# Performance work log

Measured on AMD Instinct MI355X. Metric: run time of the kernel, lower is better.

Reference implementation:

```python
import jax, jax.numpy as jnp
import numpy as np

B, S, D, H, E, K = 4, 1024, 1024, 4096, 8, 2


def setup_inputs() -> dict:
    key = jax.random.key(0)
    ks = jax.random.split(key, 5)
    std = 0.02
    return {
        "x": jax.random.normal(ks[0], (B, S, D), dtype=jnp.float32),
        "router_W": jax.random.normal(ks[1], (D, E), dtype=jnp.float32) * std,
        "W_in": jax.random.normal(ks[2], (E, D, H), dtype=jnp.float32) * std,
        "b_in": jnp.zeros((E, H), dtype=jnp.float32),
        "W_out": jax.random.normal(ks[3], (E, H, D), dtype=jnp.float32) * std,
        "b_out": jnp.zeros((E, D), dtype=jnp.float32),
    }


def reference(x, router_W, W_in, b_in, W_out, b_out):
    # ---- routing ----
    logits = jnp.einsum("bsd,de->bse", x, router_W)          # [B,S,E]
    probs = jax.nn.softmax(logits, axis=-1)                    # [B,S,E]
    top_p, top_i = jax.lax.top_k(probs, K)                     # [B,S,K]
    top_p = top_p / (jnp.sum(top_p, axis=-1, keepdims=True) + 1e-8)
    one_hot = jax.nn.one_hot(top_i, E, dtype=x.dtype)          # [B,S,K,E]
    combine = jnp.sum(one_hot * top_p[..., None], axis=-2)     # [B,S,E] per-expert weight

    # ---- experts (original runs full batch through every selected expert;
    #      with E=8, K=2 all experts are active, so run all densely) ----
    h = jnp.einsum("bsd,edh->ebsh", x, W_in) + b_in[:, None, None, :]
    h = jax.nn.gelu(h, approximate=False)
    y = jnp.einsum("ebsh,ehd->ebsd", h, W_out) + b_out[:, None, None, :]
    out = jnp.einsum("bse,ebsd->bsd", combine, y)              # weighted combine

    # ---- load-balancing aux loss ----
    expert_usage = jnp.mean(one_hot, axis=(0, 1, 2))           # f_i, fraction of routed slots
    avg_probs = jnp.mean(probs, axis=(0, 1))                   # P_i
    aux_loss = E * jnp.sum(avg_probs * expert_usage)
    return out, aux_loss
```

## Files before the change

kernel.cpp:

```cpp
#include <hip/hip_runtime.h>
#include <hip/hip_bf16.h>
#include <math.h>

#define B_ 4
#define S_ 1024
#define T_ (B_ * S_)
#define D_ 1024
#define H_ 4096
#define E_ 8
#define K_ 2
#define A_ (T_ * K_)
#define NTM_ 40

typedef __bf16 bf16x8_t __attribute__((ext_vector_type(8)));
typedef float f32x4_t __attribute__((ext_vector_type(4)));
typedef unsigned short u16x8_t __attribute__((ext_vector_type(8)));

__device__ inline unsigned short f2bf(float f) {
    __hip_bfloat16 h = __float2bfloat16(f);
    return *reinterpret_cast<unsigned short*>(&h);
}

__device__ __forceinline__ void gl2lds16(const unsigned short* g, unsigned short* l) {
    auto* gp = reinterpret_cast<const __attribute__((address_space(1))) unsigned int*>(
        reinterpret_cast<uintptr_t>(g));
    auto* lp = reinterpret_cast<__attribute__((address_space(3))) unsigned int*>(
        reinterpret_cast<uintptr_t>(l));
    __builtin_amdgcn_global_load_lds(gp, lp, 16, 0, 0);
}


__global__ void router_kernel(const float* __restrict__ x, const float* __restrict__ rw,
                              int* __restrict__ tok_e, float* __restrict__ tok_w,
                              int* __restrict__ counts_pad, float* __restrict__ probs_pad) {
    __shared__ float s_probs[E_];
    __shared__ int s_counts[E_];
    const int tid = threadIdx.x;
    if (tid < E_) { s_probs[tid] = 0.f; s_counts[tid] = 0; }
    __syncthreads();
    const int wave = tid >> 6;
    const int lane = tid & 63;

    float wprob[E_];
    int wcount[E_];
#pragma unroll
    for (int e = 0; e < E_; ++e) { wprob[e] = 0.f; wcount[e] = 0; }

    for (int tt = 0; tt < 4; ++tt) {
        const int token = blockIdx.x * 16 + wave * 4 + tt;
        const float* xr = x + (long)token * D_;
        float acc[E_];
#pragma unroll
        for (int e = 0; e < E_; ++e) acc[e] = 0.f;
        for (int i = 0; i < D_ / 64; ++i) {
            int d = i * 64 + lane;
            float xv = xr[d];
            const float* w = rw + (long)d * E_;
#pragma unroll
            for (int e = 0; e < E_; ++e) acc[e] += xv * w[e];
        }
#pragma unroll
        for (int e = 0; e < E_; ++e) {
            for (int off = 32; off > 0; off >>= 1)
                acc[e] += __shfl_down(acc[e], off);
        }
        if (lane == 0) {
            float m = acc[0];
            for (int e = 1; e < E_; ++e) m = fmaxf(m, acc[e]);
            float p[E_], s = 0.f;
            for (int e = 0; e < E_; ++e) { p[e] = expf(acc[e] - m); s += p[e]; }
            float inv = 1.f / s;
            for (int e = 0; e < E_; ++e) { p[e] *= inv; wprob[e] += p[e]; }
            int i0 = 0;
            for (int e = 1; e < E_; ++e) if (p[e] > p[i0]) i0 = e;
            int i1 = (i0 == 0) ? 1 : 0;
            for (int e = 0; e < E_; ++e) if (e != i0 && p[e] > p[i1]) i1 = e;
            float w0 = p[i0], w1 = p[i1];
            float inv2 = 1.f / (w0 + w1 + 1e-8f);
            tok_e[token * 2] = i0;
            tok_e[token * 2 + 1] = i1;
            tok_w[token * 2] = w0 * inv2;
            tok_w[token * 2 + 1] = w1 * inv2;
            wcount[i0]++; wcount[i1]++;
        }
    }
    if (lane == 0) {
#pragma unroll
        for (int e = 0; e < E_; ++e) {
            atomicAdd(&s_probs[e], wprob[e]);
            if (wcount[e]) atomicAdd(&s_counts[e], wcount[e]);
        }
    }
    __syncthreads();
    if (tid < E_) {
        atomicAdd(&probs_pad[tid * 32], s_probs[tid]);
        if (s_counts[tid]) atomicAdd(&counts_pad[tid * 32], s_counts[tid]);
    }
}

__global__ void offsets_aux_kernel(const int* __restrict__ counts_pad,
                                   const float* __restrict__ probs_pad,
                                   int* __restrict__ offsets,
                                   int* __restrict__ tile_e, int* __restrict__ tile_m,
                                   int* __restrict__ n_tiles, float* __restrict__ aux_out) {
    if (threadIdx.x == 0 && blockIdx.x == 0) {
        int run = 0, t = 0;
        for (int e = 0; e < E_; ++e) {
            int c = counts_pad[e * 32];
            offsets[e] = run;
            for (int m0 = 0; m0 < c; m0 += 256) {
                tile_e[t] = e; tile_m[t] = m0; ++t;
            }
            run += c;
        }
        offsets[E_] = run;
        *n_tiles = t;
        float aux = 0.f;
        for (int e = 0; e < E_; ++e)
            aux += (probs_pad[e * 32] / (float)T_) * ((float)counts_pad[e * 32] / (float)A_);
        *aux_out = (float)E_ * aux;
    }
}

__global__ void scatter_kernel(const int* __restrict__ tok_e, const float* __restrict__ tok_w,
                               const int* __restrict__ offsets, int* __restrict__ cursors_pad,
                               int* __restrict__ perm_token, float* __restrict__ perm_weight,
                               int* __restrict__ inv_pos) {
    int i = blockIdx.x * blockDim.x + threadIdx.x;
    int lane = threadIdx.x & 63;
    int e = tok_e[i];
    float w = tok_w[i];
    unsigned long long bal[E_];
#pragma unroll
    for (int q = 0; q < E_; ++q) bal[q] = __ballot(e == q);
    unsigned long long below = (1ull << lane) - 1ull;
    int rank = __popcll(bal[e] & below);
    int base = 0;
    if (lane < E_) {
        int c = __popcll(bal[lane]);
        if (c) base = atomicAdd(&cursors_pad[lane * 32], c);
    }
    int mybase = __shfl(base, e);
    int pos = offsets[e] + mybase + rank;
    perm_token[pos] = i >> 1;
    perm_weight[pos] = w;
    inv_pos[i] = pos;
}

__global__ void cast_x_kernel(const float* __restrict__ x, unsigned short* __restrict__ xb) {
    long i = (long)blockIdx.x * blockDim.x + threadIdx.x;
    float4 v = reinterpret_cast<const float4*>(x)[i];
    unsigned long long packed = (unsigned long long)f2bf(v.x)
        | ((unsigned long long)f2bf(v.y) << 16)
        | ((unsigned long long)f2bf(v.z) << 32)
        | ((unsigned long long)f2bf(v.w) << 48);
    reinterpret_cast<unsigned long long*>(xb)[i] = packed;
}

__global__ void transpose_cast_kernel(const float* __restrict__ in, unsigned short* __restrict__ out,
                                      int R, int C) {
    __shared__ float tile[64][65];
    const long e = blockIdx.z;
    const float* in_e = in + e * (long)R * C;
    unsigned short* out_e = out + e * (long)R * C;
    const int c0 = blockIdx.x * 64;
    const int r0 = blockIdx.y * 64;
    const int tid = threadIdx.x;
    const int c4 = (tid & 15) * 4;
    const int rb = tid >> 4;
#pragma unroll
    for (int i = 0; i < 4; ++i) {
        const int r = rb + i * 16;
        const float4 v = *reinterpret_cast<const float4*>(&in_e[(long)(r0 + r) * C + c0 + c4]);
        tile[r][c4] = v.x; tile[r][c4 + 1] = v.y; tile[r][c4 + 2] = v.z; tile[r][c4 + 3] = v.w;
    }
    __syncthreads();
    const int rs = (tid & 7) * 8;
    const int cb = tid >> 3;
#pragma unroll
    for (int i = 0; i < 2; ++i) {
        const int c = cb + i * 32;
        u16x8_t p;
#pragma unroll
        for (int j = 0; j < 8; ++j) p[j] = f2bf(tile[rs + j][c]);
        *reinterpret_cast<u16x8_t*>(&out_e[(long)(c0 + c) * R + r0 + rs]) = p;
    }
}

template <int PHASE, int NSPLIT>
__launch_bounds__(512, 2)
__global__ void moe_gemm_kernel(const unsigned short* __restrict__ A_src,
                                const unsigned short* __restrict__ B_src,
                                const float* __restrict__ bias,
                                const int* __restrict__ offsets,
                                const int* __restrict__ tile_e, const int* __restrict__ tile_m,
                                const int* __restrict__ p_ntiles,
                                const int* __restrict__ perm_token,
                                const float* __restrict__ perm_weight,
                                unsigned short* __restrict__ h_buf,
                                float* __restrict__ y_perm) {
    constexpr int Ksz  = (PHASE == 1) ? D_ : H_;
    constexpr int Kloc = (PHASE == 1) ? D_ : (H_ / NSPLIT);
    constexpr int Nsz  = (PHASE == 1) ? H_ : D_;
    constexpr int NT   = Kloc / 64;
    constexpr int NTN  = Nsz / 128;

    const int nwg = gridDim.x;
    const int id = blockIdx.x;
    const int q = nwg >> 3, r8 = nwg & 7;
    const int xcd = id & 7, sub = id >> 3;
    const int wg = (xcd < r8 ? xcd * (q + 1) : r8 * (q + 1) + (xcd - r8) * q) + sub;
    const int mt = wg % NTM_;
    if (mt >= *p_ntiles) return;
    const int rest = wg / NTM_;
    const int nt = rest % NTN;
    const int kh = rest / NTN;
    const int e = tile_e[mt];
    const int m0 = tile_m[mt];
    const int off_e = offsets[e];
    const int n_e = offsets[e + 1] - off_e;
    const int n0 = nt * 128;
    const long k_base = (long)kh * Kloc;

    __shared__ __attribute__((aligned(16))) unsigned short lds_a[3 * 256 * 64];
    __shared__ __attribute__((aligned(16))) unsigned short lds_b[3 * 128 * 64];

    const int tid = threadIdx.x;
    const int lane = tid & 63;
    const int wave = tid >> 6;
    const int wr = wave >> 1;
    const int wc = wave & 1;
    const int lrow = lane & 15;
    const int kg = lane >> 4;

    const unsigned short* gA[4];
    const unsigned short* gB[2];
    int dstA[4], dstB[2];
#pragma unroll
    for (int j = 0; j < 4; ++j) {
        const int chunk = j * 512 + tid;
        const int rr = chunk >> 3;
        const int ch = tid & 7;
        const int m_loc = m0 + rr;
        const int m_cl = (m_loc < n_e) ? m_loc : (n_e - 1);
        const int pos = off_e + m_cl;
        long arow;
        if (PHASE == 1) arow = (long)perm_token[pos] * Ksz;
        else            arow = (long)pos * Ksz;
        gA[j] = A_src + arow + k_base + ((ch ^ (rr & 7)) * 8);
        dstA[j] = (j * 512 + wave * 64) * 8;
    }
#pragma unroll
    for (int j = 0; j < 2; ++j) {
        const int chunk = j * 512 + tid;
        const int rr = chunk >> 3;
        const int ch = tid & 7;
        gB[j] = B_src + (long)e * Nsz * Ksz + (long)(n0 + rr) * Ksz + k_base + ((ch ^ (rr & 7)) * 8);
        dstB[j] = (j * 512 + wave * 64) * 8;
    }

    int aoff[2][4], boff[2][4];
#pragma unroll
    for (int kf = 0; kf < 2; ++kf)
#pragma unroll
        for (int i = 0; i < 4; ++i) {
            const int r = wr * 64 + i * 16 + lrow;
            aoff[kf][i] = r * 64 + (((kf * 4 + kg) ^ (r & 7)) * 8);
            const int c = wc * 64 + i * 16 + lrow;
            boff[kf][i] = c * 64 + (((kf * 4 + kg) ^ (c & 7)) * 8);
        }

    f32x4_t acc[4][4];
#pragma unroll
    for (int i = 0; i < 4; ++i)
#pragma unroll
        for (int j = 0; j < 4; ++j) acc[i][j] = (f32x4_t){0.f, 0.f, 0.f, 0.f};

#pragma unroll
    for (int tt = 0; tt < 2; ++tt) {
        gl2lds16(gA[0] + tt * 64, lds_a + tt * 16384 + dstA[0]);
        gl2lds16(gA[1] + tt * 64, lds_a + tt * 16384 + dstA[1]);
        gl2lds16(gB[0] + tt * 64, lds_b + tt * 8192 + dstB[0]);
        gl2lds16(gA[2] + tt * 64, lds_a + tt * 16384 + dstA[2]);
        gl2lds16(gA[3] + tt * 64, lds_a + tt * 16384 + dstA[3]);
        gl2lds16(gB[1] + tt * 64, lds_b + tt * 8192 + dstB[1]);
    }
    asm volatile("s_waitcnt vmcnt(6)" ::: "memory");
    __builtin_amdgcn_s_barrier();

    for (int t = 0; t < NT; ++t) {
        const int s = t % 3;
        const int s2 = (t + 2) % 3;
        const unsigned short* la = lds_a + s * 16384;
        const unsigned short* lb = lds_b + s * 8192;
        const bool pf = (t + 2 < NT);

        bf16x8_t a0[4], b0[4];
#pragma unroll
        for (int i = 0; i < 4; ++i) a0[i] = *reinterpret_cast<const bf16x8_t*>(la + aoff[0][i]);
#pragma unroll
        for (int i = 0; i < 4; ++i) b0[i] = *reinterpret_cast<const bf16x8_t*>(lb + boff[0][i]);
        if (pf) {
            gl2lds16(gA[0] + (t + 2) * 64, lds_a + s2 * 16384 + dstA[0]);
            gl2lds16(gA[1] + (t + 2) * 64, lds_a + s2 * 16384 + dstA[1]);
            gl2lds16(gB[0] + (t + 2) * 64, lds_b + s2 * 8192 + dstB[0]);
        }
        __builtin_amdgcn_s_barrier();
        asm volatile("s_waitcnt lgkmcnt(0)" ::: "memory");
        __builtin_amdgcn_sched_barrier(0);
        __builtin_amdgcn_s_setprio(1);
#pragma unroll
        for (int i = 0; i < 4; ++i)
#pragma unroll
            for (int j = 0; j < 4; ++j)
                acc[i][j] = __builtin_amdgcn_mfma_f32_16x16x32_bf16(a0[i], b0[j], acc[i][j], 0, 0, 0);
        __builtin_amdgcn_s_setprio(0);
        __builtin_amdgcn_s_barrier();

        bf16x8_t a1[4], b1[4];
#pragma unroll
        for (int i = 0; i < 4; ++i) a1[i] = *reinterpret_cast<const bf16x8_t*>(la + aoff[1][i]);
#pragma unroll
        for (int i = 0; i < 4; ++i) b1[i] = *reinterpret_cast<const bf16x8_t*>(lb + boff[1][i]);
        if (pf) {
            gl2lds16(gA[2] + (t + 2) * 64, lds_a + s2 * 16384 + dstA[2]);
            gl2lds16(gA[3] + (t + 2) * 64, lds_a + s2 * 16384 + dstA[3]);
            gl2lds16(gB[1] + (t + 2) * 64, lds_b + s2 * 8192 + dstB[1]);
        }
        __builtin_amdgcn_s_barrier();
        asm volatile("s_waitcnt lgkmcnt(0)" ::: "memory");
        __builtin_amdgcn_sched_barrier(0);
        __builtin_amdgcn_s_setprio(1);
#pragma unroll
        for (int i = 0; i < 4; ++i)
#pragma unroll
            for (int j = 0; j < 4; ++j)
                acc[i][j] = __builtin_amdgcn_mfma_f32_16x16x32_bf16(a1[i], b1[j], acc[i][j], 0, 0, 0);
        __builtin_amdgcn_s_setprio(0);
        if (t + 1 < NT) {
            if (t + 2 < NT) asm volatile("s_waitcnt vmcnt(6)" ::: "memory");
            else            asm volatile("s_waitcnt vmcnt(0)" ::: "memory");
        }
        __builtin_amdgcn_s_barrier();
    }

    const float* bias_e = bias + (long)e * Nsz;
    if (PHASE == 1) {
#pragma unroll
        for (int i = 0; i < 4; ++i) {
#pragma unroll
            for (int rq = 0; rq < 4; ++rq) {
                const int row_loc = wr * 64 + i * 16 + kg * 4 + rq;
                const int m_loc = m0 + row_loc;
                if (m_loc >= n_e) continue;
                const int pos = off_e + m_loc;
#pragma unroll
                for (int j = 0; j < 4; ++j) {
                    const int n = n0 + wc * 64 + j * 16 + lrow;
                    float v = acc[i][j][rq] + bias_e[n];
                    v = 0.5f * v * (1.0f + erff(v * 0.70710678118654752440f));
                    h_buf[(long)pos * Nsz + n] = f2bf(v);
                }
            }
        }
    } else {
        float* yp = y_perm + (long)kh * ((long)A_ * D_);
#pragma unroll
        for (int i = 0; i < 4; ++i) {
#pragma unroll
            for (int rq = 0; rq < 4; ++rq) {
                const int row_loc = wr * 64 + i * 16 + kg * 4 + rq;
                const int m_loc = m0 + row_loc;
                if (m_loc >= n_e) continue;
                const int pos = off_e + m_loc;
                const float wgt = perm_weight[pos];
#pragma unroll
                for (int j = 0; j < 4; ++j) {
                    const int n = n0 + wc * 64 + j * 16 + lrow;
                    float v = acc[i][j][rq] + ((kh == 0) ? bias_e[n] : 0.f);
                    yp[(long)pos * Nsz + n] = v * wgt;
                }
            }
        }
    }
}

__global__ void combine_kernel(const float* __restrict__ y_perm, const int* __restrict__ inv_pos,
                               float* __restrict__ out, int splitk) {
    int t = blockIdx.x;
    int d4 = threadIdx.x;
    int p0 = inv_pos[t * 2];
    int p1 = inv_pos[t * 2 + 1];
    const float4* y0 = reinterpret_cast<const float4*>(y_perm);
    float4 a = y0[(long)p0 * (D_ / 4) + d4];
    float4 b = y0[(long)p1 * (D_ / 4) + d4];
    float4 o = {a.x + b.x, a.y + b.y, a.z + b.z, a.w + b.w};
    if (splitk) {
        const float4* y1 = reinterpret_cast<const float4*>(y_perm + (long)A_ * D_);
        float4 c = y1[(long)p0 * (D_ / 4) + d4];
        float4 d = y1[(long)p1 * (D_ / 4) + d4];
        o.x += c.x + d.x; o.y += c.y + d.y; o.z += c.z + d.z; o.w += c.w + d.w;
    }
    reinterpret_cast<float4*>(out + (long)t * D_)[d4] = o;
}

extern "C" void kernel_launch(void* const* d_in, const int* in_sizes, int n_in,
                              void* d_out, int out_size, void* d_ws, size_t ws_size,
                              hipStream_t stream) {
    const float* x        = (const float*)d_in[0];
    const float* router_W = (const float*)d_in[1];
    const float* W_in     = (const float*)d_in[2];
    const float* b_in     = (const float*)d_in[3];
    const float* W_out    = (const float*)d_in[4];
    const float* b_out    = (const float*)d_in[5];
    float* out = (float*)d_out;

    char* ws = (char*)d_ws;
    size_t off = 0;
    auto alloc = [&](size_t bytes) -> void* {
        void* p = ws + off;
        off += (bytes + 255) & ~(size_t)255;
        return p;
    };

    const int splitk = (ws_size >= (size_t)290 * 1024 * 1024) ? 1 : 0;

    char* ctrl = (char*)alloc(4096);
    int* counts_pad   = (int*)ctrl;
    float* probs_pad  = (float*)(ctrl + 1024);
    int* cursors_pad  = (int*)(ctrl + 2048);
    int* offsets      = (int*)(ctrl + 3072);
    int* tile_e       = (int*)(ctrl + 3200);
    int* tile_m       = (int*)(ctrl + 3584);
    int* n_tiles      = (int*)(ctrl + 3968);
    int* tok_e         = (int*)alloc((size_t)A_ * 4);
    float* tok_w       = (float*)alloc((size_t)A_ * 4);
    int* perm_token    = (int*)alloc((size_t)A_ * 4);
    float* perm_weight = (float*)alloc((size_t)A_ * 4);
    int* inv_pos       = (int*)alloc((size_t)A_ * 4);
    unsigned short* x_bf    = (unsigned short*)alloc((size_t)T_ * D_ * 2);
    unsigned short* w_in_t  = (unsigned short*)alloc((size_t)E_ * D_ * H_ * 2);
    unsigned short* w_out_t = (unsigned short*)alloc((size_t)E_ * D_ * H_ * 2);
    unsigned short* h_buf   = (unsigned short*)alloc((size_t)A_ * H_ * 2);
    float* y_perm           = (float*)alloc((size_t)(1 + splitk) * A_ * D_ * 4);

    hipMemsetAsync(ctrl, 0, 4096, stream);

    cast_x_kernel<<<(T_ * D_ / 4) / 256, 256, 0, stream>>>(x, x_bf);
    transpose_cast_kernel<<<dim3(H_ / 64, D_ / 64, E_), 256, 0, stream>>>(W_in, w_in_t, D_, H_);
    transpose_cast_kernel<<<dim3(D_ / 64, H_ / 64, E_), 256, 0, stream>>>(W_out, w_out_t, H_, D_);
    router_kernel<<<T_ / 16, 256, 0, stream>>>(x, router_W, tok_e, tok_w, counts_pad, probs_pad);
    offsets_aux_kernel<<<1, 64, 0, stream>>>(counts_pad, probs_pad, offsets,
                                             tile_e, tile_m, n_tiles, out + (out_size - 1));
    scatter_kernel<<<A_ / 256, 256, 0, stream>>>(tok_e, tok_w, offsets, cursors_pad,
                                                 perm_token, perm_weight, inv_pos);

    moe_gemm_kernel<1, 1><<<NTM_ * (H_ / 128), 512, 0, stream>>>(
        x_bf, w_in_t, b_in, offsets, tile_e, tile_m, n_tiles,
        perm_token, perm_weight, h_buf, y_perm);
    if (splitk) {
        moe_gemm_kernel<2, 2><<<NTM_ * (D_ / 128) * 2, 512, 0, stream>>>(
            h_buf, w_out_t, b_out, offsets, tile_e, tile_m, n_tiles,
            perm_token, perm_weight, h_buf, y_perm);
    } else {
        moe_gemm_kernel<2, 1><<<NTM_ * (D_ / 128), 512, 0, stream>>>(
            h_buf, w_out_t, b_out, offsets, tile_e, tile_m, n_tiles,
            perm_token, perm_weight, h_buf, y_perm);
    }
    combine_kernel<<<T_, 256, 0, stream>>>(y_perm, inv_pos, out, splitk);
}
```

Before: 682.7 us.

## Widen GEMM N-tile to 256 with 32-wide K stages and new LDS swizzle

The MoE GEMM kernel is templated on the N-tile width. Both phases now use 256x256 output tiles, with waves arranged 2x4 instead of 4x2, while the split-K=1 fallback keeps 128. The K step per pipeline stage drops from 64 to 32, which halves the triple-buffered LDS footprint, and it uses a new XOR swizzle with per-wave 16-row load groups. Several intra-iteration barriers are removed, so one barrier per K step remains. The aim is more reuse of A and B per block and less synchronisation. The cost is twice as many K iterations, higher accumulator register pressure, and a slightly lower workspace threshold for split-K.

```diff
diff --git a/kernel.cpp b/kernel.cpp
--- a/kernel.cpp
+++ b/kernel.cpp
@@ -28,7 +28,6 @@
         reinterpret_cast<uintptr_t>(l));
     __builtin_amdgcn_global_load_lds(gp, lp, 16, 0, 0);
 }
-
 
 __global__ void router_kernel(const float* __restrict__ x, const float* __restrict__ rw,
                               int* __restrict__ tok_e, float* __restrict__ tok_w,
@@ -187,7 +186,7 @@
     }
 }
 
-template <int PHASE, int NSPLIT>
+template <int PHASE, int BN_, int NSPLIT>
 __launch_bounds__(512, 2)
 __global__ void moe_gemm_kernel(const unsigned short* __restrict__ A_src,
                                 const unsigned short* __restrict__ B_src,
@@ -200,10 +199,20 @@
                                 unsigned short* __restrict__ h_buf,
                                 float* __restrict__ y_perm) {
     constexpr int Ksz  = (PHASE == 1) ? D_ : H_;
-    constexpr int Kloc = (PHASE == 1) ? D_ : (H_ / NSPLIT);
+    constexpr int Kloc = Ksz / NSPLIT;
     constexpr int Nsz  = (PHASE == 1) ? H_ : D_;
-    constexpr int NT   = Kloc / 64;
-    constexpr int NTN  = Nsz / 128;
+    constexpr int NT   = Kloc / 32;
+    constexpr int NTN  = Nsz / BN_;
+    constexpr int WN   = BN_ / 64;
+    constexpr int WM   = 8 / WN;
+    constexpr int MROWS = 256 / WM;
+    constexpr int MF   = MROWS / 16;
+    constexpr int MH   = MF / 2;
+    constexpr int AI   = 2;
+    constexpr int BI   = BN_ / 128;
+    constexpr int SI   = AI + BI;
+    constexpr int ABUF = 256 * 32;
+    constexpr int BBUF = BN_ * 32;
 
     const int nwg = gridDim.x;
     const int id = blockIdx.x;
@@ -219,138 +228,118 @@
     const int m0 = tile_m[mt];
     const int off_e = offsets[e];
     const int n_e = offsets[e + 1] - off_e;
-    const int n0 = nt * 128;
+    const int n0 = nt * BN_;
     const long k_base = (long)kh * Kloc;
 
-    __shared__ __attribute__((aligned(16))) unsigned short lds_a[3 * 256 * 64];
-    __shared__ __attribute__((aligned(16))) unsigned short lds_b[3 * 128 * 64];
+    __shared__ __attribute__((aligned(16))) unsigned short lds_a[3 * ABUF];
+    __shared__ __attribute__((aligned(16))) unsigned short lds_b[3 * BBUF];
 
     const int tid = threadIdx.x;
     const int lane = tid & 63;
     const int wave = tid >> 6;
-    const int wr = wave >> 1;
-    const int wc = wave & 1;
+    const int wr = wave / WN;
+    const int wc = wave % WN;
     const int lrow = lane & 15;
     const int kg = lane >> 4;
 
-    const unsigned short* gA[4];
-    const unsigned short* gB[2];
-    int dstA[4], dstB[2];
-#pragma unroll
-    for (int j = 0; j < 4; ++j) {
-        const int chunk = j * 512 + tid;
-        const int rr = chunk >> 3;
-        const int ch = tid & 7;
-        const int m_loc = m0 + rr;
+    const int srow = lane >> 2;
+    const int sch  = (lane & 3) ^ ((lane >> 3) & 3);
+    const unsigned short* gA[AI];
+    const unsigned short* gB[BI];
+#pragma unroll
+    for (int j = 0; j < AI; ++j) {
+        const int g = wave * AI + j;
+        const int m_loc = m0 + g * 16 + srow;
         const int m_cl = (m_loc < n_e) ? m_loc : (n_e - 1);
         const int pos = off_e + m_cl;
         long arow;
         if (PHASE == 1) arow = (long)perm_token[pos] * Ksz;
         else            arow = (long)pos * Ksz;
-        gA[j] = A_src + arow + k_base + ((ch ^ (rr & 7)) * 8);
-        dstA[j] = (j * 512 + wave * 64) * 8;
-    }
-#pragma unroll
-    for (int j = 0; j < 2; ++j) {
-        const int chunk = j * 512 + tid;
-        const int rr = chunk >> 3;
-        const int ch = tid & 7;
-        gB[j] = B_src + (long)e * Nsz * Ksz + (long)(n0 + rr) * Ksz + k_base + ((ch ^ (rr & 7)) * 8);
-        dstB[j] = (j * 512 + wave * 64) * 8;
-    }
-
-    int aoff[2][4], boff[2][4];
-#pragma unroll
-    for (int kf = 0; kf < 2; ++kf)
-#pragma unroll
-        for (int i = 0; i < 4; ++i) {
-            const int r = wr * 64 + i * 16 + lrow;
-            aoff[kf][i] = r * 64 + (((kf * 4 + kg) ^ (r & 7)) * 8);
-            const int c = wc * 64 + i * 16 + lrow;
-            boff[kf][i] = c * 64 + (((kf * 4 + kg) ^ (c & 7)) * 8);
-        }
-
-    f32x4_t acc[4][4];
-#pragma unroll
-    for (int i = 0; i < 4; ++i)
+        gA[j] = A_src + arow + k_base + sch * 8;
+    }
+#pragma unroll
+    for (int j = 0; j < BI; ++j) {
+        const int g = wave * BI + j;
+        gB[j] = B_src + (long)e * Nsz * Ksz + (long)(n0 + g * 16 + srow) * Ksz + k_base + sch * 8;
+    }
+
+    const int rch = (kg ^ ((lrow >> 1) & 3)) * 8;
+    const int abase = (wr * MROWS + lrow) * 32 + rch;
+    const int bbase = (wc * 64 + lrow) * 32 + rch;
+
+    f32x4_t acc[MF][4];
+#pragma unroll
+    for (int i = 0; i < MF; ++i)
 #pragma unroll
         for (int j = 0; j < 4; ++j) acc[i][j] = (f32x4_t){0.f, 0.f, 0.f, 0.f};
 
 #pragma unroll
     for (int tt = 0; tt < 2; ++tt) {
-        gl2lds16(gA[0] + tt * 64, lds_a + tt * 16384 + dstA[0]);
-        gl2lds16(gA[1] + tt * 64, lds_a + tt * 16384 + dstA[1]);
-        gl2lds16(gB[0] + tt * 64, lds_b + tt * 8192 + dstB[0]);
-        gl2lds16(gA[2] + tt * 64, lds_a + tt * 16384 + dstA[2]);
-        gl2lds16(gA[3] + tt * 64, lds_a + tt * 16384 + dstA[3]);
-        gl2lds16(gB[1] + tt * 64, lds_b + tt * 8192 + dstB[1]);
-    }
-    asm volatile("s_waitcnt vmcnt(6)" ::: "memory");
+#pragma unroll
+        for (int j = 0; j < AI; ++j)
+            gl2lds16(gA[j] + tt * 32, lds_a + tt * ABUF + (wave * AI + j) * 512);
+#pragma unroll
+        for (int j = 0; j < BI; ++j)
+            gl2lds16(gB[j] + tt * 32, lds_b + tt * BBUF + (wave * BI + j) * 512);
+    }
+    if constexpr (SI == 4) asm volatile("s_waitcnt vmcnt(4)" ::: "memory");
+    else                   asm volatile("s_waitcnt vmcnt(3)" ::: "memory");
     __builtin_amdgcn_s_barrier();
 
+    int s = 0;
     for (int t = 0; t < NT; ++t) {
-        const int s = t % 3;
-        const int s2 = (t + 2) % 3;
-        const unsigned short* la = lds_a + s * 16384;
-        const unsigned short* lb = lds_b + s * 8192;
+        const int s2 = (s + 2 >= 3) ? s - 1 : s + 2;
+        const unsigned short* la = lds_a + s * ABUF;
+        const unsigned short* lb = lds_b + s * BBUF;
         const bool pf = (t + 2 < NT);
 
-        bf16x8_t a0[4], b0[4];
-#pragma unroll
-        for (int i = 0; i < 4; ++i) a0[i] = *reinterpret_cast<const bf16x8_t*>(la + aoff[0][i]);
-#pragma unroll
-        for (int i = 0; i < 4; ++i) b0[i] = *reinterpret_cast<const bf16x8_t*>(lb + boff[0][i]);
-        if (pf) {
-            gl2lds16(gA[0] + (t + 2) * 64, lds_a + s2 * 16384 + dstA[0]);
-            gl2lds16(gA[1] + (t + 2) * 64, lds_a + s2 * 16384 + dstA[1]);
-            gl2lds16(gB[0] + (t + 2) * 64, lds_b + s2 * 8192 + dstB[0]);
-        }
-        __builtin_amdgcn_s_barrier();
-        asm volatile("s_waitcnt lgkmcnt(0)" ::: "memory");
-        __builtin_amdgcn_sched_barrier(0);
-        __builtin_amdgcn_s_setprio(1);
-#pragma unroll
-        for (int i = 0; i < 4; ++i)
-#pragma unroll
-            for (int j = 0; j < 4; ++j)
-                acc[i][j] = __builtin_amdgcn_mfma_f32_16x16x32_bf16(a0[i], b0[j], acc[i][j], 0, 0, 0);
-        __builtin_amdgcn_s_setprio(0);
-        __builtin_amdgcn_s_barrier();
-
-        bf16x8_t a1[4], b1[4];
-#pragma unroll
-        for (int i = 0; i < 4; ++i) a1[i] = *reinterpret_cast<const bf16x8_t*>(la + aoff[1][i]);
-#pragma unroll
-        for (int i = 0; i < 4; ++i) b1[i] = *reinterpret_cast<const bf16x8_t*>(lb + boff[1][i]);
-        if (pf) {
-            gl2lds16(gA[2] + (t + 2) * 64, lds_a + s2 * 16384 + dstA[2]);
-            gl2lds16(gA[3] + (t + 2) * 64, lds_a + s2 * 16384 + dstA[3]);
-            gl2lds16(gB[1] + (t + 2) * 64, lds_b + s2 * 8192 + dstB[1]);
-        }
-        __builtin_amdgcn_s_barrier();
-        asm volatile("s_waitcnt lgkmcnt(0)" ::: "memory");
-        __builtin_amdgcn_sched_barrier(0);
-        __builtin_amdgcn_s_setprio(1);
-#pragma unroll
-        for (int i = 0; i < 4; ++i)
-#pragma unroll
-            for (int j = 0; j < 4; ++j)
-                acc[i][j] = __builtin_amdgcn_mfma_f32_16x16x32_bf16(a1[i], b1[j], acc[i][j], 0, 0, 0);
-        __builtin_amdgcn_s_setprio(0);
+        bf16x8_t b_frag[4];
+#pragma unroll
+        for (int p = 0; p < 2; ++p) {
+            bf16x8_t a_frag[MH];
+#pragma unroll
+            for (int f = 0; f < MH; ++f)
+                a_frag[f] = *reinterpret_cast<const bf16x8_t*>(la + abase + (p * MH + f) * 512);
+            if (p == 0) {
+#pragma unroll
+                for (int j = 0; j < 4; ++j)
+                    b_frag[j] = *reinterpret_cast<const bf16x8_t*>(lb + bbase + j * 512);
+            }
+            if (pf) {
+                gl2lds16(gA[p] + (t + 2) * 32, lds_a + s2 * ABUF + (wave * AI + p) * 512);
+                if (p < BI)
+                    gl2lds16(gB[p] + (t + 2) * 32, lds_b + s2 * BBUF + (wave * BI + p) * 512);
+            }
+            asm volatile("s_waitcnt lgkmcnt(0)" ::: "memory");
+            __builtin_amdgcn_sched_barrier(0);
+            __builtin_amdgcn_s_setprio(1);
+#pragma unroll
+            for (int f = 0; f < MH; ++f)
+#pragma unroll
+                for (int j = 0; j < 4; ++j)
+                    acc[p * MH + f][j] = __builtin_amdgcn_mfma_f32_16x16x32_bf16(
+                        a_frag[f], b_frag[j], acc[p * MH + f][j], 0, 0, 0);
+            __builtin_amdgcn_s_setprio(0);
+        }
         if (t + 1 < NT) {
-            if (t + 2 < NT) asm volatile("s_waitcnt vmcnt(6)" ::: "memory");
-            else            asm volatile("s_waitcnt vmcnt(0)" ::: "memory");
-        }
-        __builtin_amdgcn_s_barrier();
+            if (pf) {
+                if constexpr (SI == 4) asm volatile("s_waitcnt vmcnt(4)" ::: "memory");
+                else                   asm volatile("s_waitcnt vmcnt(3)" ::: "memory");
+            } else {
+                asm volatile("s_waitcnt vmcnt(0)" ::: "memory");
+            }
+            __builtin_amdgcn_s_barrier();
+        }
+        s = (s + 1 >= 3) ? 0 : s + 1;
     }
 
     const float* bias_e = bias + (long)e * Nsz;
     if (PHASE == 1) {
 #pragma unroll
-        for (int i = 0; i < 4; ++i) {
+        for (int i = 0; i < MF; ++i) {
 #pragma unroll
             for (int rq = 0; rq < 4; ++rq) {
-                const int row_loc = wr * 64 + i * 16 + kg * 4 + rq;
+                const int row_loc = wr * MROWS + i * 16 + kg * 4 + rq;
                 const int m_loc = m0 + row_loc;
                 if (m_loc >= n_e) continue;
                 const int pos = off_e + m_loc;
@@ -366,10 +355,10 @@
     } else {
         float* yp = y_perm + (long)kh * ((long)A_ * D_);
 #pragma unroll
-        for (int i = 0; i < 4; ++i) {
+        for (int i = 0; i < MF; ++i) {
 #pragma unroll
             for (int rq = 0; rq < 4; ++rq) {
-                const int row_loc = wr * 64 + i * 16 + kg * 4 + rq;
+                const int row_loc = wr * MROWS + i * 16 + kg * 4 + rq;
                 const int m_loc = m0 + row_loc;
                 if (m_loc >= n_e) continue;
                 const int pos = off_e + m_loc;
@@ -423,7 +412,7 @@
         return p;
     };
 
-    const int splitk = (ws_size >= (size_t)290 * 1024 * 1024) ? 1 : 0;
+    const int splitk = (ws_size >= (size_t)280 * 1024 * 1024) ? 1 : 0;
 
     char* ctrl = (char*)alloc(4096);
     int* counts_pad   = (int*)ctrl;
@@ -455,15 +444,15 @@
     scatter_kernel<<<A_ / 256, 256, 0, stream>>>(tok_e, tok_w, offsets, cursors_pad,
                                                  perm_token, perm_weight, inv_pos);
 
-    moe_gemm_kernel<1, 1><<<NTM_ * (H_ / 128), 512, 0, stream>>>(
+    moe_gemm_kernel<1, 256, 1><<<NTM_ * (H_ / 256), 512, 0, stream>>>(
         x_bf, w_in_t, b_in, offsets, tile_e, tile_m, n_tiles,
         perm_token, perm_weight, h_buf, y_perm);
     if (splitk) {
-        moe_gemm_kernel<2, 2><<<NTM_ * (D_ / 128) * 2, 512, 0, stream>>>(
+        moe_gemm_kernel<2, 256, 2><<<NTM_ * (D_ / 256) * 2, 512, 0, stream>>>(
             h_buf, w_out_t, b_out, offsets, tile_e, tile_m, n_tiles,
             perm_token, perm_weight, h_buf, y_perm);
     } else {
-        moe_gemm_kernel<2, 1><<<NTM_ * (D_ / 128), 512, 0, stream>>>(
+        moe_gemm_kernel<2, 128, 1><<<NTM_ * (D_ / 128), 512, 0, stream>>>(
             h_buf, w_out_t, b_out, offsets, tile_e, tile_m, n_tiles,
             perm_token, perm_weight, h_buf, y_perm);
     }
```

Result: no change. 678.3 us (-0.7%).

## Retile MoE GEMM to 256x256 blocks with 1024 threads and 4-stage pipeline

Applied to the files above, without the earlier changes.

Restructures the grouped expert GEMM: block tile becomes 256x256 with 16 waves (1024 threads), K-step shrinks to 32, and the LDS ring grows to 4 stages with one barrier per step instead of several. This raises data reuse per block and simplifies synchronisation. The change also replaces the erff GELU with a polynomial erf approximation and adds a 4-way split-K option for the second GEMM when workspace allows. The risks are higher register pressure under launch_bounds(1024,4), fewer blocks to fill the GPU, and small numerical deviation from the GELU approximation.

```diff
diff --git a/kernel.cpp b/kernel.cpp
--- a/kernel.cpp
+++ b/kernel.cpp
@@ -21,6 +21,18 @@
     return *reinterpret_cast<unsigned short*>(&h);
 }
 
+__device__ __forceinline__ float fast_gelu(float v) {
+    float z = v * 0.70710678118654752440f;
+    float az = fabsf(z);
+    float t = __builtin_amdgcn_rcpf(1.0f + 0.3275911f * az);
+    float poly = ((((1.061405429f * t - 1.453152027f) * t + 1.421413741f) * t
+                   - 0.284496736f) * t + 0.254829592f) * t;
+    float e = __expf(-az * az);
+    float erfv = 1.0f - poly * e;
+    erfv = (z < 0.0f) ? -erfv : erfv;
+    return 0.5f * v * (1.0f + erfv);
+}
+
 __device__ __forceinline__ void gl2lds16(const unsigned short* g, unsigned short* l) {
     auto* gp = reinterpret_cast<const __attribute__((address_space(1))) unsigned int*>(
         reinterpret_cast<uintptr_t>(g));
@@ -28,7 +40,6 @@
         reinterpret_cast<uintptr_t>(l));
     __builtin_amdgcn_global_load_lds(gp, lp, 16, 0, 0);
 }
-
 
 __global__ void router_kernel(const float* __restrict__ x, const float* __restrict__ rw,
                               int* __restrict__ tok_e, float* __restrict__ tok_w,
@@ -188,8 +199,7 @@
 }
 
 template <int PHASE, int NSPLIT>
-__launch_bounds__(512, 2)
-__global__ void moe_gemm_kernel(const unsigned short* __restrict__ A_src,
+__device__ __forceinline__ void gemm_body(const unsigned short* __restrict__ A_src,
                                 const unsigned short* __restrict__ B_src,
                                 const float* __restrict__ bias,
                                 const int* __restrict__ offsets,
@@ -200,10 +210,10 @@
                                 unsigned short* __restrict__ h_buf,
                                 float* __restrict__ y_perm) {
     constexpr int Ksz  = (PHASE == 1) ? D_ : H_;
-    constexpr int Kloc = (PHASE == 1) ? D_ : (H_ / NSPLIT);
+    constexpr int Kloc = Ksz / NSPLIT;
     constexpr int Nsz  = (PHASE == 1) ? H_ : D_;
-    constexpr int NT   = Kloc / 64;
-    constexpr int NTN  = Nsz / 128;
+    constexpr int NT   = Kloc / 32;
+    constexpr int NTN  = Nsz / 256;
 
     const int nwg = gridDim.x;
     const int id = blockIdx.x;
@@ -219,93 +229,72 @@
     const int m0 = tile_m[mt];
     const int off_e = offsets[e];
     const int n_e = offsets[e + 1] - off_e;
-    const int n0 = nt * 128;
+    const int n0 = nt * 256;
     const long k_base = (long)kh * Kloc;
 
-    __shared__ __attribute__((aligned(16))) unsigned short lds_a[3 * 256 * 64];
-    __shared__ __attribute__((aligned(16))) unsigned short lds_b[3 * 128 * 64];
+    __shared__ __attribute__((aligned(16))) unsigned short lds_a[4 * 8192];
+    __shared__ __attribute__((aligned(16))) unsigned short lds_b[4 * 8192];
 
     const int tid = threadIdx.x;
     const int lane = tid & 63;
     const int wave = tid >> 6;
-    const int wr = wave >> 1;
-    const int wc = wave & 1;
+    const int wr = wave >> 2;
+    const int wc = wave & 3;
     const int lrow = lane & 15;
     const int kg = lane >> 4;
 
-    const unsigned short* gA[4];
-    const unsigned short* gB[2];
-    int dstA[4], dstB[2];
-#pragma unroll
-    for (int j = 0; j < 4; ++j) {
-        const int chunk = j * 512 + tid;
-        const int rr = chunk >> 3;
-        const int ch = tid & 7;
-        const int m_loc = m0 + rr;
-        const int m_cl = (m_loc < n_e) ? m_loc : (n_e - 1);
-        const int pos = off_e + m_cl;
-        long arow;
-        if (PHASE == 1) arow = (long)perm_token[pos] * Ksz;
-        else            arow = (long)pos * Ksz;
-        gA[j] = A_src + arow + k_base + ((ch ^ (rr & 7)) * 8);
-        dstA[j] = (j * 512 + wave * 64) * 8;
-    }
-#pragma unroll
-    for (int j = 0; j < 2; ++j) {
-        const int chunk = j * 512 + tid;
-        const int rr = chunk >> 3;
-        const int ch = tid & 7;
-        gB[j] = B_src + (long)e * Nsz * Ksz + (long)(n0 + rr) * Ksz + k_base + ((ch ^ (rr & 7)) * 8);
-        dstB[j] = (j * 512 + wave * 64) * 8;
-    }
-
-    int aoff[2][4], boff[2][4];
-#pragma unroll
-    for (int kf = 0; kf < 2; ++kf)
+    const int srow = lane >> 2;
+    const int grow = wave * 16 + srow;
+    const int sc = (lane & 3) ^ ((grow >> 1) & 3);
+    const int m_loc = m0 + grow;
+    const int m_cl = (m_loc < n_e) ? m_loc : (n_e - 1);
+    const int spos = off_e + m_cl;
+    long arow;
+    if (PHASE == 1) arow = (long)perm_token[spos] * Ksz;
+    else            arow = (long)spos * Ksz;
+    const unsigned short* gA = A_src + arow + k_base + sc * 8;
+    const unsigned short* gB = B_src + (long)e * Nsz * Ksz + (long)(n0 + grow) * Ksz + k_base + sc * 8;
+    unsigned short* const la0 = lds_a + wave * 512;
+    unsigned short* const lb0 = lds_b + wave * 512;
+
+    int aoff[4], boff[4];
+#pragma unroll
+    for (int i = 0; i < 4; ++i) {
+        const int r = wr * 64 + i * 16 + lrow;
+        aoff[i] = r * 32 + ((kg ^ ((r >> 1) & 3)) * 8);
+        const int c = wc * 64 + i * 16 + lrow;
+        boff[i] = c * 32 + ((kg ^ ((c >> 1) & 3)) * 8);
+    }
+
+    f32x4_t acc[4][4];
+#pragma unroll
+    for (int i = 0; i < 4; ++i)
+#pragma unroll
+        for (int j = 0; j < 4; ++j) acc[i][j] = (f32x4_t){0.f, 0.f, 0.f, 0.f};
+
+#pragma unroll
+    for (int tt = 0; tt < 3; ++tt) {
+        gl2lds16(gA + tt * 32, la0 + tt * 8192);
+        gl2lds16(gB + tt * 32, lb0 + tt * 8192);
+    }
+
+    for (int t = 0; t < NT; ++t) {
+        if (t + 2 < NT)      asm volatile("s_waitcnt vmcnt(4)" ::: "memory");
+        else if (t + 1 < NT) asm volatile("s_waitcnt vmcnt(2)" ::: "memory");
+        else                 asm volatile("s_waitcnt vmcnt(0)" ::: "memory");
+        __builtin_amdgcn_s_barrier();
+        if (t + 3 < NT) {
+            gl2lds16(gA + (t + 3) * 32, la0 + ((t + 3) & 3) * 8192);
+            gl2lds16(gB + (t + 3) * 32, lb0 + ((t + 3) & 3) * 8192);
+        }
+        const unsigned short* la = lds_a + (t & 3) * 8192;
+        const unsigned short* lb = lds_b + (t & 3) * 8192;
+        bf16x8_t af[4], bf[4];
 #pragma unroll
         for (int i = 0; i < 4; ++i) {
-            const int r = wr * 64 + i * 16 + lrow;
-            aoff[kf][i] = r * 64 + (((kf * 4 + kg) ^ (r & 7)) * 8);
-            const int c = wc * 64 + i * 16 + lrow;
-            boff[kf][i] = c * 64 + (((kf * 4 + kg) ^ (c & 7)) * 8);
-        }
-
-    f32x4_t acc[4][4];
-#pragma unroll
-    for (int i = 0; i < 4; ++i)
-#pragma unroll
-        for (int j = 0; j < 4; ++j) acc[i][j] = (f32x4_t){0.f, 0.f, 0.f, 0.f};
-
-#pragma unroll
-    for (int tt = 0; tt < 2; ++tt) {
-        gl2lds16(gA[0] + tt * 64, lds_a + tt * 16384 + dstA[0]);
-        gl2lds16(gA[1] + tt * 64, lds_a + tt * 16384 + dstA[1]);
-        gl2lds16(gB[0] + tt * 64, lds_b + tt * 8192 + dstB[0]);
-        gl2lds16(gA[2] + tt * 64, lds_a + tt * 16384 + dstA[2]);
-        gl2lds16(gA[3] + tt * 64, lds_a + tt * 16384 + dstA[3]);
-        gl2lds16(gB[1] + tt * 64, lds_b + tt * 8192 + dstB[1]);
-    }
-    asm volatile("s_waitcnt vmcnt(6)" ::: "memory");
-    __builtin_amdgcn_s_barrier();
-
-    for (int t = 0; t < NT; ++t) {
-        const int s = t % 3;
-        const int s2 = (t + 2) % 3;
-        const unsigned short* la = lds_a + s * 16384;
-        const unsigned short* lb = lds_b + s * 8192;
-        const bool pf = (t + 2 < NT);
-
-        bf16x8_t a0[4], b0[4];
-#pragma unroll
-        for (int i = 0; i < 4; ++i) a0[i] = *reinterpret_cast<const bf16x8_t*>(la + aoff[0][i]);
-#pragma unroll
-        for (int i = 0; i < 4; ++i) b0[i] = *reinterpret_cast<const bf16x8_t*>(lb + boff[0][i]);
-        if (pf) {
-            gl2lds16(gA[0] + (t + 2) * 64, lds_a + s2 * 16384 + dstA[0]);
-            gl2lds16(gA[1] + (t + 2) * 64, lds_a + s2 * 16384 + dstA[1]);
-            gl2lds16(gB[0] + (t + 2) * 64, lds_b + s2 * 8192 + dstB[0]);
-        }
-        __builtin_amdgcn_s_barrier();
+            af[i] = *reinterpret_cast<const bf16x8_t*>(la + aoff[i]);
+            bf[i] = *reinterpret_cast<const bf16x8_t*>(lb + boff[i]);
+        }
         asm volatile("s_waitcnt lgkmcnt(0)" ::: "memory");
         __builtin_amdgcn_sched_barrier(0);
         __builtin_amdgcn_s_setprio(1);
@@ -313,66 +302,28 @@
         for (int i = 0; i < 4; ++i)
 #pragma unroll
             for (int j = 0; j < 4; ++j)
-                acc[i][j] = __builtin_amdgcn_mfma_f32_16x16x32_bf16(a0[i], b0[j], acc[i][j], 0, 0, 0);
+                acc[i][j] = __builtin_amdgcn_mfma_f32_16x16x32_bf16(af[i], bf[j], acc[i][j], 0, 0, 0);
         __builtin_amdgcn_s_setprio(0);
-        __builtin_amdgcn_s_barrier();
-
-        bf16x8_t a1[4], b1[4];
-#pragma unroll
-        for (int i = 0; i < 4; ++i) a1[i] = *reinterpret_cast<const bf16x8_t*>(la + aoff[1][i]);
-#pragma unroll
-        for (int i = 0; i < 4; ++i) b1[i] = *reinterpret_cast<const bf16x8_t*>(lb + boff[1][i]);
-        if (pf) {
-            gl2lds16(gA[2] + (t + 2) * 64, lds_a + s2 * 16384 + dstA[2]);
-            gl2lds16(gA[3] + (t + 2) * 64, lds_a + s2 * 16384 + dstA[3]);
-            gl2lds16(gB[1] + (t + 2) * 64, lds_b + s2 * 8192 + dstB[1]);
-        }
-        __builtin_amdgcn_s_barrier();
-        asm volatile("s_waitcnt lgkmcnt(0)" ::: "memory");
-        __builtin_amdgcn_sched_barrier(0);
-        __builtin_amdgcn_s_setprio(1);
-#pragma unroll
-        for (int i = 0; i < 4; ++i)
-#pragma unroll
-            for (int j = 0; j < 4; ++j)
-                acc[i][j] = __builtin_amdgcn_mfma_f32_16x16x32_bf16(a1[i], b1[j], acc[i][j], 0, 0, 0);
-        __builtin_amdgcn_s_setprio(0);
-        if (t + 1 < NT) {
-            if (t + 2 < NT) asm volatile("s_waitcnt vmcnt(6)" ::: "memory");
-            else            asm volatile("s_waitcnt vmcnt(0)" ::: "memory");
-        }
-        __builtin_amdgcn_s_barrier();
     }
 
     const float* bias_e = bias + (long)e * Nsz;
-    if (PHASE == 1) {
-#pragma unroll
-        for (int i = 0; i < 4; ++i) {
-#pragma unroll
-            for (int rq = 0; rq < 4; ++rq) {
-                const int row_loc = wr * 64 + i * 16 + kg * 4 + rq;
-                const int m_loc = m0 + row_loc;
-                if (m_loc >= n_e) continue;
-                const int pos = off_e + m_loc;
+#pragma unroll
+    for (int i = 0; i < 4; ++i) {
+#pragma unroll
+        for (int rq = 0; rq < 4; ++rq) {
+            const int row_loc = wr * 64 + i * 16 + kg * 4 + rq;
+            const int m_out = m0 + row_loc;
+            if (m_out >= n_e) continue;
+            const int pos = off_e + m_out;
+            if (PHASE == 1) {
 #pragma unroll
                 for (int j = 0; j < 4; ++j) {
                     const int n = n0 + wc * 64 + j * 16 + lrow;
                     float v = acc[i][j][rq] + bias_e[n];
-                    v = 0.5f * v * (1.0f + erff(v * 0.70710678118654752440f));
-                    h_buf[(long)pos * Nsz + n] = f2bf(v);
+                    h_buf[(long)pos * Nsz + n] = f2bf(fast_gelu(v));
                 }
-            }
-        }
-    } else {
-        float* yp = y_perm + (long)kh * ((long)A_ * D_);
-#pragma unroll
-        for (int i = 0; i < 4; ++i) {
-#pragma unroll
-            for (int rq = 0; rq < 4; ++rq) {
-                const int row_loc = wr * 64 + i * 16 + kg * 4 + rq;
-                const int m_loc = m0 + row_loc;
-                if (m_loc >= n_e) continue;
-                const int pos = off_e + m_loc;
+            } else {
+                float* yp = y_perm + (long)kh * ((long)A_ * D_);
                 const float wgt = perm_weight[pos];
 #pragma unroll
                 for (int j = 0; j < 4; ++j) {
@@ -385,21 +336,40 @@
     }
 }
 
+#define GEMM_ARGS const unsigned short* __restrict__ A_src, \
+                  const unsigned short* __restrict__ B_src, \
+                  const float* __restrict__ bias, \
+                  const int* __restrict__ offsets, \
+                  const int* __restrict__ tile_e, const int* __restrict__ tile_m, \
+                  const int* __restrict__ p_ntiles, \
+                  const int* __restrict__ perm_token, \
+                  const float* __restrict__ perm_weight, \
+                  unsigned short* __restrict__ h_buf, \
+                  float* __restrict__ y_perm
+#define GEMM_PASS A_src, B_src, bias, offsets, tile_e, tile_m, p_ntiles, \
+                  perm_token, perm_weight, h_buf, y_perm
+
+__launch_bounds__(1024, 4)
+__global__ void moe_gemm_p1(GEMM_ARGS) { gemm_body<1, 1>(GEMM_PASS); }
+__launch_bounds__(1024, 4)
+__global__ void moe_gemm_p2s1(GEMM_ARGS) { gemm_body<2, 1>(GEMM_PASS); }
+__launch_bounds__(1024, 4)
+__global__ void moe_gemm_p2s2(GEMM_ARGS) { gemm_body<2, 2>(GEMM_PASS); }
+__launch_bounds__(1024, 4)
+__global__ void moe_gemm_p2s4(GEMM_ARGS) { gemm_body<2, 4>(GEMM_PASS); }
+
 __global__ void combine_kernel(const float* __restrict__ y_perm, const int* __restrict__ inv_pos,
-                               float* __restrict__ out, int splitk) {
+                               float* __restrict__ out, int ns) {
     int t = blockIdx.x;
     int d4 = threadIdx.x;
     int p0 = inv_pos[t * 2];
     int p1 = inv_pos[t * 2 + 1];
-    const float4* y0 = reinterpret_cast<const float4*>(y_perm);
-    float4 a = y0[(long)p0 * (D_ / 4) + d4];
-    float4 b = y0[(long)p1 * (D_ / 4) + d4];
-    float4 o = {a.x + b.x, a.y + b.y, a.z + b.z, a.w + b.w};
-    if (splitk) {
-        const float4* y1 = reinterpret_cast<const float4*>(y_perm + (long)A_ * D_);
-        float4 c = y1[(long)p0 * (D_ / 4) + d4];
-        float4 d = y1[(long)p1 * (D_ / 4) + d4];
-        o.x += c.x + d.x; o.y += c.y + d.y; o.z += c.z + d.z; o.w += c.w + d.w;
+    float4 o = {0.f, 0.f, 0.f, 0.f};
+    for (int s = 0; s < ns; ++s) {
+        const float4* y = reinterpret_cast<const float4*>(y_perm + (long)s * A_ * D_);
+        float4 a = y[(long)p0 * (D_ / 4) + d4];
+        float4 b = y[(long)p1 * (D_ / 4) + d4];
+        o.x += a.x + b.x; o.y += a.y + b.y; o.z += a.z + b.z; o.w += a.w + b.w;
     }
     reinterpret_cast<float4*>(out + (long)t * D_)[d4] = o;
 }
@@ -423,7 +393,9 @@
         return p;
     };
 
-    const int splitk = (ws_size >= (size_t)290 * 1024 * 1024) ? 1 : 0;
+    int ns = 1;
+    if (ws_size >= (size_t)340 * 1024 * 1024)      ns = 4;
+    else if (ws_size >= (size_t)272 * 1024 * 1024) ns = 2;
 
     char* ctrl = (char*)alloc(4096);
     int* counts_pad   = (int*)ctrl;
@@ -442,7 +414,7 @@
     unsigned short* w_in_t  = (unsigned short*)alloc((size_t)E_ * D_ * H_ * 2);
     unsigned short* w_out_t = (unsigned short*)alloc((size_t)E_ * D_ * H_ * 2);
     unsigned short* h_buf   = (unsigned short*)alloc((size_t)A_ * H_ * 2);
-    float* y_perm           = (float*)alloc((size_t)(1 + splitk) * A_ * D_ * 4);
+    float* y_perm           = (float*)alloc((size_t)ns * A_ * D_ * 4);
 
     hipMemsetAsync(ctrl, 0, 4096, stream);
 
@@ -455,17 +427,21 @@
     scatter_kernel<<<A_ / 256, 256, 0, stream>>>(tok_e, tok_w, offsets, cursors_pad,
                                                  perm_token, perm_weight, inv_pos);
 
-    moe_gemm_kernel<1, 1><<<NTM_ * (H_ / 128), 512, 0, stream>>>(
+    moe_gemm_p1<<<NTM_ * (H_ / 256), 1024, 0, stream>>>(
         x_bf, w_in_t, b_in, offsets, tile_e, tile_m, n_tiles,
         perm_token, perm_weight, h_buf, y_perm);
-    if (splitk) {
-        moe_gemm_kernel<2, 2><<<NTM_ * (D_ / 128) * 2, 512, 0, stream>>>(
+    if (ns == 4) {
+        moe_gemm_p2s4<<<NTM_ * (D_ / 256) * 4, 1024, 0, stream>>>(
+            h_buf, w_out_t, b_out, offsets, tile_e, tile_m, n_tiles,
+            perm_token, perm_weight, h_buf, y_perm);
+    } else if (ns == 2) {
+        moe_gemm_p2s2<<<NTM_ * (D_ / 256) * 2, 1024, 0, stream>>>(
             h_buf, w_out_t, b_out, offsets, tile_e, tile_m, n_tiles,
             perm_token, perm_weight, h_buf, y_perm);
     } else {
-        moe_gemm_kernel<2, 1><<<NTM_ * (D_ / 128), 512, 0, stream>>>(
+        moe_gemm_p2s1<<<NTM_ * (D_ / 256), 1024, 0, stream>>>(
             h_buf, w_out_t, b_out, offsets, tile_e, tile_m, n_tiles,
             perm_token, perm_weight, h_buf, y_perm);
     }
-    combine_kernel<<<T_, 256, 0, stream>>>(y_perm, inv_pos, out, splitk);
-}
+    combine_kernel<<<T_, 256, 0, stream>>>(y_perm, inv_pos, out, ns);
+}
```

New measurement: 634.9 us. -7.0%, faster.
